# Performance work log

Measured on AMD Instinct MI355X. Metric: run time of the kernel, lower is better.

## Reference

```python
import jax, jax.numpy as jnp
import numpy as np

B, T, C = 2, 2048, 2048
H = 16
HS = C // H           # 128
ROT = HS // 2         # 64 partial-rotary dims
BASE = 10000.0


def setup_inputs() -> dict:
    key = jax.random.key(0)
    ks = jax.random.split(key, 9)
    s = 1.0 / np.sqrt(C)
    return {
        "x": jax.random.normal(ks[0], (B, T, C), jnp.float32),
        "Wq": jax.random.normal(ks[1], (C, C), jnp.float32) * s,
        "bq": jax.random.normal(ks[2], (C,), jnp.float32) * 0.02,
        "Wk": jax.random.normal(ks[3], (C, C), jnp.float32) * s,
        "bk": jax.random.normal(ks[4], (C,), jnp.float32) * 0.02,
        "Wv": jax.random.normal(ks[5], (C, C), jnp.float32) * s,
        "bv": jax.random.normal(ks[6], (C,), jnp.float32) * 0.02,
        "Wo": jax.random.normal(ks[7], (C, C), jnp.float32) * s,
        "bo": jax.random.normal(ks[8], (C,), jnp.float32) * 0.02,
    }


def _rotate_half(u):
    u1, u2 = u[..., : u.shape[-1] // 2], u[..., u.shape[-1] // 2 :]
    return jnp.concatenate((-u2, u1), axis=-1)


def _rope_tables(t_len):
    inv_freq = 1.0 / (BASE ** (jnp.arange(0, ROT, 2, dtype=jnp.float32) / ROT))
    freqs = jnp.arange(t_len, dtype=jnp.float32)[:, None] * inv_freq[None, :]
    emb = jnp.concatenate((freqs, freqs), axis=-1)  # [T, ROT]
    return jnp.cos(emb), jnp.sin(emb)


def reference(x, Wq, bq, Wk, bk, Wv, bv, Wo, bo):
    Bs, Ts, Cs = x.shape
    q = (x @ Wq.T + bq).reshape(Bs, Ts, H, HS).transpose(0, 2, 1, 3)  # [B,H,T,HS]
    k = (x @ Wk.T + bk).reshape(Bs, Ts, H, HS).transpose(0, 2, 1, 3)
    v = (x @ Wv.T + bv).reshape(Bs, Ts, H, HS).transpose(0, 2, 1, 3)

    # partial rotary on first ROT dims of each head
    cos, sin = _rope_tables(Ts)  # [T, ROT] broadcast over B,H
    q_rot, q_pass = q[..., :ROT], q[..., ROT:]
    k_rot, k_pass = k[..., :ROT], k[..., ROT:]
    q_rot = q_rot * cos + _rotate_half(q_rot) * sin
    k_rot = k_rot * cos + _rotate_half(k_rot) * sin
    q = jnp.concatenate((q_rot, q_pass), axis=-1)
    k = jnp.concatenate((k_rot, k_pass), axis=-1)

    att = jnp.einsum("bhqd,bhkd->bhqk", q, k) * (1.0 / np.sqrt(HS))
    causal = jnp.tril(jnp.ones((Ts, Ts), dtype=bool))
    att = jnp.where(causal, att, jnp.float32(-jnp.inf))
    att = jax.nn.softmax(att, axis=-1)
    out = jnp.einsum("bhqk,bhkd->bhqd", att, v)          # [B,H,T,HS]
    out = out.transpose(0, 2, 1, 3).reshape(Bs, Ts, Cs)  # [B,T,C]
    return out @ Wo.T + bo
```

## Files before the change

### kernel.cpp

```cpp
#include <hip/hip_runtime.h>
#include <hip/hip_bf16.h>

#define Bdim 2
#define Tdim 2048
#define Cdim 2048
#define Hn   16

using bf16x8 = __attribute__((ext_vector_type(8))) short;
using f32x4  = __attribute__((ext_vector_type(4))) float;
using f32x16 = __attribute__((ext_vector_type(16))) float;
typedef __hip_bfloat16 bf16;

#define VMWAIT(n) asm volatile("s_waitcnt vmcnt(" #n ")" ::: "memory")
#define CROW(r, hi) (((r) & 3) + 8 * ((r) >> 2) + 4 * (hi))
#define QS2 ((float)(0.08838834764831845 * 1.4426950408889634))
#define THR2 11.5415603f

__device__ __forceinline__ void load_lds16(const void* g, void* l) {
  __builtin_amdgcn_global_load_lds(
      (const __attribute__((address_space(1))) void*)g,
      (__attribute__((address_space(3))) void*)l, 16, 0, 0);
}

__device__ __forceinline__ float bf2f(unsigned short u) {
  union { unsigned int i; float f; } x; x.i = ((unsigned int)u) << 16; return x.f;
}
__device__ __forceinline__ unsigned short f2bf(float f) {
  bf16 h = __float2bfloat16(f); return *(unsigned short*)&h;
}
__device__ __forceinline__ unsigned cvtpk(float lo, float hi) {
  unsigned r;
  asm volatile("v_cvt_pk_bf16_f32 %0, %1, %2" : "=v"(r) : "v"(lo), "v"(hi));
  return r;
}

__global__ __launch_bounds__(256) void cvt_all(const float* __restrict__ x,
                                               const float* __restrict__ w0,
                                               const float* __restrict__ w1,
                                               const float* __restrict__ w2,
                                               const float* __restrict__ w3,
                                               bf16* __restrict__ dx,
                                               bf16* __restrict__ d0,
                                               bf16* __restrict__ d1,
                                               bf16* __restrict__ d2,
                                               bf16* __restrict__ d3) {
  const int NX = (Bdim * Tdim * Cdim) / 4;
  const int NW = (Cdim * Cdim) / 4;
  int i = blockIdx.x * 256 + threadIdx.x;
  int stride = gridDim.x * 256;
  for (; i < NX + 4 * NW; i += stride) {
    const float* s; bf16* d; int j;
    if (i < NX) { s = x; d = dx; j = i; }
    else {
      int k = i - NX;
      int wsel = k >> 20;
      j = k & (NW - 1);
      s = wsel == 0 ? w0 : wsel == 1 ? w1 : wsel == 2 ? w2 : w3;
      d = wsel == 0 ? d0 : wsel == 1 ? d1 : wsel == 2 ? d2 : d3;
    }
    float4 v = ((const float4*)s)[j];
    ushort4 o;
    o.x = f2bf(v.x); o.y = f2bf(v.y); o.z = f2bf(v.z); o.w = f2bf(v.w);
    ((ushort4*)d)[j] = o;
  }
}

__global__ __launch_bounds__(256) void rope_tables_k(float2* __restrict__ cst) {
  int idx = blockIdx.x * blockDim.x + threadIdx.x;
  if (idx >= Tdim * 32) return;
  int t = idx >> 5, i = idx & 31;
  double f = pow(10000.0, -(double)i / 32.0);
  double ang = (double)t * f;
  cst[idx] = make_float2((float)cos(ang), (float)sin(ang));
}

__global__ __launch_bounds__(512, 2) void gemmQKV(
    const bf16* __restrict__ A, const bf16* __restrict__ Wcat,
    const float* __restrict__ b0, const float* __restrict__ b1, const float* __restrict__ b2,
    bf16* __restrict__ oq, bf16* __restrict__ ok, bf16* __restrict__ vt,
    const float2* __restrict__ cst) {
  extern __shared__ char lds[];
  const int tid = threadIdx.x, lane = tid & 63, wid = tid >> 6;
  const int l31 = lane & 31, hi = lane >> 5;
  const int wr = wid >> 2, wc = wid & 3;
  const int wbase = wid * 1024;

  const int q8 = gridDim.x >> 3;
  const int swz = ((int)blockIdx.x & 7) * q8 + ((int)blockIdx.x >> 3);
  const int bm = (swz >> 4) * 256;
  const int strip = swz & 15;

  const int rS = tid >> 2, sS = tid & 3;
  const int ssw = (sS ^ ((rS >> 1) & 3)) << 3;
  const bf16* thrA = A + (size_t)(bm + rS) * 2048 + ssw;
  const bf16* thrB = Wcat + (size_t)(strip * 384 + rS) * 2048 + ssw;

#define SA(T, DB) { load_lds16(thrA + (T) * 32, (DB) + wbase);                              \
                    load_lds16(thrA + (size_t)128 * 2048 + (T) * 32, (DB) + 8192 + wbase); }
#define SB(T, DB) { load_lds16(thrB + (T) * 32, (DB) + 16384 + wbase);                      \
                    load_lds16(thrB + (size_t)128 * 2048 + (T) * 32, (DB) + 24576 + wbase); \
                    load_lds16(thrB + (size_t)256 * 2048 + (T) * 32, (DB) + 32768 + wbase); }

  f32x16 acc[4][3] = {};
  bf16x8 afr[4], bfr[3];
  const int q2 = (l31 >> 1) & 3;
  const int aoff = (wr * 128 + l31) * 64;
  const int boff = 16384 + (wc * 96 + l31) * 64;
  const int sl0 = (hi ^ q2) << 4;
  const int sl1 = sl0 ^ 32;

#define READF(PB, SL)                                                        \
  {                                                                          \
    const char* _p = (PB);                                                   \
    _Pragma("unroll")                                                        \
    for (int m_ = 0; m_ < 4; ++m_)                                           \
      afr[m_] = *(const bf16x8*)(_p + aoff + m_ * 2048 + (SL));              \
    _Pragma("unroll")                                                        \
    for (int n_ = 0; n_ < 3; ++n_)                                           \
      bfr[n_] = *(const bf16x8*)(_p + boff + n_ * 2048 + (SL));              \
  }

#define MF12()                                                               \
  __builtin_amdgcn_s_setprio(1);                                             \
  _Pragma("unroll")                                                          \
  for (int m_ = 0; m_ < 4; ++m_)                                             \
    _Pragma("unroll")                                                        \
    for (int n_ = 0; n_ < 3; ++n_)                                           \
      acc[m_][n_] = __builtin_amdgcn_mfma_f32_32x32x16_bf16(                 \
          afr[m_], bfr[n_], acc[m_][n_], 0, 0, 0);                           \
  __builtin_amdgcn_s_setprio(0);

#define BARS()                                                               \
  __builtin_amdgcn_s_barrier();                                              \
  asm volatile("s_waitcnt lgkmcnt(0)" ::: "memory");                         \
  __builtin_amdgcn_sched_barrier(0);

#define BARE() __builtin_amdgcn_s_barrier();

  SA(0, lds); SB(0, lds);
  SA(1, lds + 40960); SB(1, lds + 40960);
  VMWAIT(5);
  __builtin_amdgcn_s_barrier();

  const char* rb = lds;
  char* sb = lds + 81920;
  const int NT = 64;

  for (int t = 0; t < NT - 2; ++t) {
    READF(rb, sl0);
    SA(t + 2, sb);
    BARS(); MF12(); BARE();
    READF(rb, sl1);
    SB(t + 2, sb);
    VMWAIT(5);
    BARS(); MF12(); BARE();
    rb = (rb == lds + 81920) ? lds : rb + 40960;
    sb = (sb == lds + 81920) ? lds : sb + 40960;
  }
  {
    READF(rb, sl0);
    BARS(); MF12(); BARE();
    READF(rb, sl1);
    VMWAIT(0);
    BARS(); MF12(); BARE();
    rb = (rb == lds + 81920) ? lds : rb + 40960;
  }
  {
    READF(rb, sl0);
    BARS(); MF12(); BARE();
    READF(rb, sl1);
    BARS(); MF12(); BARE();
  }

  __syncthreads();
  if (wc == 3) {
    const int col0 = strip * 384 + 288;
    const int mat = col0 >> 11;
    if (mat < 2) {
      const int oc0 = col0 & 2047;
      const float bv = (mat == 0 ? b0 : b1)[oc0 + l31];
      #pragma unroll
      for (int m = 0; m < 4; ++m)
        #pragma unroll
        for (int g = 0; g < 4; ++g) {
          f32x4 v;
          v[0] = acc[m][0][4 * g + 0] + bv;
          v[1] = acc[m][0][4 * g + 1] + bv;
          v[2] = acc[m][0][4 * g + 2] + bv;
          v[3] = acc[m][0][4 * g + 3] + bv;
          *(f32x4*)(lds + (((((wr * 4 + m) * 4 + g) * 2 + hi) * 32) + l31) * 16) = v;
        }
    }
  }
  __syncthreads();

  #pragma unroll
  for (int m = 0; m < 4; ++m) {
    const int rowb = bm + wr * 128 + m * 32;
    const int bb = rowb >> 11, tb = rowb & 2047;
    #pragma unroll
    for (int n = 0; n < 3; ++n) {
      const int col0 = strip * 384 + wc * 96 + n * 32;
      const int mat = col0 >> 11;
      const int oc0 = col0 & 2047;
      const float bv = (mat == 0 ? b0 : mat == 1 ? b1 : b2)[oc0 + l31];
      if (mat == 2) {
        const int hh = oc0 >> 7;
        bf16* dst = vt + ((size_t)((bb * 16 + hh) * 128 + (oc0 & 127) + l31)) * 2048 + tb;
        #pragma unroll
        for (int g = 0; g < 4; ++g) {
          ushort4 pk;
          pk.x = f2bf(acc[m][n][4 * g + 0] + bv);
          pk.y = f2bf(acc[m][n][4 * g + 1] + bv);
          pk.z = f2bf(acc[m][n][4 * g + 2] + bv);
          pk.w = f2bf(acc[m][n][4 * g + 3] + bv);
          *(ushort4*)(dst + g * 8 + hi * 4) = pk;
        }
      } else {
        const float qs = (mat == 0) ? QS2 : 1.0f;
        bf16* obf = (mat == 0) ? oq : ok;
        const int hb = (wc * 3 + n) & 3;
        if (hb == 0) {
          if (wc == 2 && n == 2) {
            #pragma unroll
            for (int g = 0; g < 4; ++g) {
              f32x4 ux = *(const f32x4*)(lds + (((((wr * 4 + m) * 4 + g) * 2 + hi) * 32) + l31) * 16);
              #pragma unroll
              for (int j = 0; j < 4; ++j) {
                const int r = 4 * g + j;
                const int row = rowb + j + 8 * g + 4 * hi;
                const int tt = row & 2047;
                float2 cs = cst[tt * 32 + l31];
                float u0 = acc[m][n][r] + bv;
                float u1 = ux[j];
                obf[(size_t)row * 2048 + oc0 + l31] =
                    __float2bfloat16((u0 * cs.x - u1 * cs.y) * qs);
                obf[(size_t)row * 2048 + oc0 + 32 + l31] =
                    __float2bfloat16((u1 * cs.x + u0 * cs.y) * qs);
              }
            }
          } else {
            const float bv1 = (mat == 0 ? b0 : b1)[oc0 + 32 + l31];
            #pragma unroll
            for (int r = 0; r < 16; ++r) {
              const int row = rowb + (r & 3) + 8 * (r >> 2) + 4 * hi;
              const int tt = row & 2047;
              float2 cs = cst[tt * 32 + l31];
              float u0 = acc[m][n][r] + bv;
              float u1 = acc[m][n + 1][r] + bv1;
              obf[(size_t)row * 2048 + oc0 + l31] =
                  __float2bfloat16((u0 * cs.x - u1 * cs.y) * qs);
              obf[(size_t)row * 2048 + oc0 + 32 + l31] =
                  __float2bfloat16((u1 * cs.x + u0 * cs.y) * qs);
            }
          }
        } else if (hb >= 2) {
          #pragma unroll
          for (int r = 0; r < 16; ++r) {
            const int row = rowb + (r & 3) + 8 * (r >> 2) + 4 * hi;
            obf[(size_t)row * 2048 + oc0 + l31] =
                __float2bfloat16((acc[m][n][r] + bv) * qs);
          }
        }
      }
    }
  }
#undef SA
#undef SB
#undef READF
#undef MF12
#undef BARS
#undef BARE
}

__global__ __launch_bounds__(512, 2) void gemmWo(
    const bf16* __restrict__ A, const bf16* __restrict__ W0,
    const float* __restrict__ b0, float* __restrict__ out, int K, int nby) {
  extern __shared__ char lds[];
  const int tid = threadIdx.x, lane = tid & 63, wid = tid >> 6;
  const int l15 = lane & 15, lhi = lane >> 4;
  const int wr = wid >> 2, wc = wid & 3;
  const int fb = (wc & 1) | ((wc >> 1) << 2);

  const int q8 = gridDim.x >> 3;
  const int swz = ((int)blockIdx.x & 7) * q8 + ((int)blockIdx.x >> 3);
  const int bm = (swz / nby) * 128, bn = (swz % nby) * 256;
  const bf16* Asrc = A + (size_t)bm * K;
  const bf16* Wsrc = W0 + (size_t)bn * K;

  const bf16 *sA0, *sA1, *sB00, *sB01, *sB10, *sB11;
  {
    int c = tid, r = c >> 3, sl = c & 7;
    size_t off = (size_t)r * K + ((sl ^ (r & 7)) << 3);
    sA0 = Asrc + off;
    sA1 = Asrc + (size_t)64 * K + off;
    sB00 = Wsrc + off;
    sB10 = Wsrc + (size_t)128 * K + off;
  }
  {
    int c = 512 + tid, r = c >> 3, sl = c & 7;
    size_t off = (size_t)r * K + ((sl ^ (r & 7)) << 3);
    sB01 = Wsrc + off;
    sB11 = Wsrc + (size_t)128 * K + off;
  }
  const int ldsA = wid * 1024;

#define SA0(t) load_lds16(sA0 + (t) * 64, lds + ((t) & 1) * 49152 + ldsA)
#define SA1(t) load_lds16(sA1 + (t) * 64, lds + ((t) & 1) * 49152 + 8192 + ldsA)
#define SB0(t) { load_lds16(sB00 + (t) * 64, lds + ((t) & 1) * 49152 + 16384 + ldsA); \
                 load_lds16(sB01 + (t) * 64, lds + ((t) & 1) * 49152 + 24576 + ldsA); }
#define SB1(t) { load_lds16(sB10 + (t) * 64, lds + ((t) & 1) * 49152 + 32768 + ldsA); \
                 load_lds16(sB11 + (t) * 64, lds + ((t) & 1) * 49152 + 40960 + ldsA); }

  f32x4 acc[4][4] = {};
  const int NT = K / 64;
  const int NI = NT / 2;
  const int asw = (l15 & 7) << 4;
  bf16x8 afr[2][2], bfr0[2][2], bfr1[2][2];

#define READ_A(BASE)                                                            \
  _Pragma("unroll")                                                             \
  for (int ii = 0; ii < 2; ++ii)                                                \
    _Pragma("unroll")                                                           \
    for (int kk = 0; kk < 2; ++kk)                                              \
      afr[ii][kk] = *(const bf16x8*)((BASE) + (wr * 32 + ii * 16 + l15) * 128   \
                                     + ((kk * 64 + lhi * 16) ^ asw));

#define READ_B(BASE, DST)                                                       \
  _Pragma("unroll")                                                             \
  for (int j = 0; j < 2; ++j)                                                   \
    _Pragma("unroll")                                                           \
    for (int kk = 0; kk < 2; ++kk)                                              \
      DST[j][kk] = *(const bf16x8*)((BASE) + ((fb + 2 * j) * 16 + l15) * 128    \
                                    + ((kk * 64 + lhi * 16) ^ asw));

#define MFMA_Q(MH, NH, BF)                                                      \
  __builtin_amdgcn_s_setprio(1);                                                \
  _Pragma("unroll")                                                             \
  for (int ii = 0; ii < 2; ++ii)                                                \
    _Pragma("unroll")                                                           \
    for (int j = 0; j < 2; ++j)                                                 \
      _Pragma("unroll")                                                         \
      for (int kk = 0; kk < 2; ++kk)                                            \
        acc[(MH) * 2 + ii][(NH) * 2 + j] =                                      \
            __builtin_amdgcn_mfma_f32_16x16x32_bf16(                            \
                afr[ii][kk], BF[j][kk], acc[(MH) * 2 + ii][(NH) * 2 + j], 0, 0, 0); \
  __builtin_amdgcn_s_setprio(0);

#define BAR_IN()                                                                \
  __builtin_amdgcn_s_barrier();                                                 \
  asm volatile("s_waitcnt lgkmcnt(0)" ::: "memory");                            \
  __builtin_amdgcn_sched_barrier(0);

#define BAR_OUT() __builtin_amdgcn_s_barrier();

  SA0(0); SB0(0); SB1(0); SA1(0);
  SA0(1); SB0(1); SB1(1);
  VMWAIT(5);
  __builtin_amdgcn_s_barrier();

  char* const buf0 = lds;
  char* const buf1 = lds + 49152;

  for (int i = 0; i < NI; ++i) {
    const int t0 = 2 * i, t1 = t0 + 1;
    const bool lastI = (i == NI - 1);

    READ_A(buf0);
    READ_B(buf0 + 16384, bfr0);
    SA1(t1);
    BAR_IN(); MFMA_Q(0, 0, bfr0); BAR_OUT();

    READ_B(buf0 + 32768, bfr1);
    if (!lastI) SA0(t0 + 2);
    BAR_IN(); MFMA_Q(0, 1, bfr1); BAR_OUT();

    READ_A(buf0 + 8192);
    if (!lastI) SB0(t0 + 2);
    BAR_IN(); MFMA_Q(1, 0, bfr0); BAR_OUT();

    if (!lastI) { SB1(t0 + 2); VMWAIT(5); } else VMWAIT(0);
    BAR_IN(); MFMA_Q(1, 1, bfr1); BAR_OUT();

    READ_A(buf1);
    READ_B(buf1 + 16384, bfr0);
    if (!lastI) SA1(t0 + 2);
    BAR_IN(); MFMA_Q(0, 0, bfr0); BAR_OUT();

    READ_B(buf1 + 32768, bfr1);
    if (!lastI) SA0(t1 + 2);
    BAR_IN(); MFMA_Q(0, 1, bfr1); BAR_OUT();

    READ_A(buf1 + 8192);
    if (!lastI) SB0(t1 + 2);
    BAR_IN(); MFMA_Q(1, 0, bfr0); BAR_OUT();

    if (!lastI) { SB1(t1 + 2); VMWAIT(5); }
    BAR_IN(); MFMA_Q(1, 1, bfr1); BAR_OUT();
  }

  #pragma unroll
  for (int mi = 0; mi < 4; ++mi) {
    const int row = bm + (mi >> 1) * 64 + wr * 32 + (mi & 1) * 16 + lhi * 4;
    #pragma unroll
    for (int nj = 0; nj < 4; ++nj) {
      const int col = bn + (nj >> 1) * 128 + (fb + 2 * (nj & 1)) * 16 + l15;
      const float bv = b0[col];
      #pragma unroll
      for (int r = 0; r < 4; ++r)
        out[(size_t)(row + r) * 2048 + col] = acc[mi][nj][r] + bv;
    }
  }
#undef SA0
#undef SA1
#undef SB0
#undef SB1
#undef READ_A
#undef READ_B
#undef MFMA_Q
#undef BAR_IN
#undef BAR_OUT
}

__global__ __launch_bounds__(256, 2) void attn_kernel(const bf16* __restrict__ Q,
                                                      const bf16* __restrict__ Kb,
                                                      const bf16* __restrict__ Vt,
                                                      bf16* __restrict__ O) {
  extern __shared__ char lds[];
  const int tid = threadIdx.x, lane = tid & 63, wave = tid >> 6;
  const int l31 = lane & 31, hi = lane >> 5;
  const int hi16 = hi << 4;

  const int bid = blockIdx.x;
  const int half = bid >> 8;
  const int idx = bid & 255;
  const int g = idx >> 5;
  const int qt = half ? g : (15 - g);
  const int bh = idx & 31;
  const int b = bh >> 4, h = bh & 15;
  const size_t bT = (size_t)b * Tdim;

  const int qb = qt * 128 + wave * 32;
  const int myq = qb + l31;

  bf16x8 qf[8];
  {
    const bf16* qrow = Q + (bT + myq) * Cdim + h * 128;
    #pragma unroll
    for (int ds = 0; ds < 8; ++ds)
      qf[ds] = *(const bf16x8*)(qrow + ds * 16 + hi * 8);
  }

  auto stageKV = [&](int kt) {
    const int k0 = kt * 64;
    char* kb = lds + (kt & 1) * 16384;
    char* vb = lds + 32768 + (kt & 1) * 16384;
    #pragma unroll
    for (int i = 0; i < 4; ++i) {
      int cb = i * 256 + wave * 64;
      int c = cb + lane;
      {
        int row = c >> 4, slot = c & 15;
        load_lds16(Kb + (bT + k0 + row) * Cdim + h * 128 + ((slot ^ (row & 7)) << 3),
                   kb + cb * 16);
      }
      {
        int row = c >> 3, slot = c & 7;
        load_lds16(Vt + ((size_t)(bh * 128 + row)) * Tdim + k0 + ((slot ^ (row & 7)) << 3),
                   vb + cb * 16);
      }
    }
  };

  f32x16 o[4] = {};
  float mrun = -1e30f, lrun = 0.f;

  const int nt = 2 * (qt + 1);
  stageKV(0);

  for (int kt = 0; kt < nt; ++kt) {
    if (kt + 1 < nt) { stageKV(kt + 1); VMWAIT(8); } else { VMWAIT(0); }
    __syncthreads();
    const char* kbuf = lds + (kt & 1) * 16384;
    const char* vbuf = lds + 32768 + (kt & 1) * 16384;
    const int k0 = kt * 64;

    const bool active = (k0 <= qb + 31);
    if (active) {
      f32x16 s0 = {}, s1 = {};
      const int krow0 = l31, krow1 = 32 + l31;
      const int ksw = (l31 & 7) << 4;
      __builtin_amdgcn_s_setprio(1);
      #pragma unroll
      for (int ds = 0; ds < 8; ++ds) {
        const int boff = (ds * 32 + hi16) ^ ksw;
        bf16x8 kf0 = *(const bf16x8*)(kbuf + krow0 * 256 + boff);
        bf16x8 kf1 = *(const bf16x8*)(kbuf + krow1 * 256 + boff);
        s0 = __builtin_amdgcn_mfma_f32_32x32x16_bf16(kf0, qf[ds], s0, 0, 0, 0);
        s1 = __builtin_amdgcn_mfma_f32_32x32x16_bf16(kf1, qf[ds], s1, 0, 0, 0);
      }
      __builtin_amdgcn_s_setprio(0);

      if (k0 + 63 > qb) {
        #pragma unroll
        for (int r = 0; r < 16; ++r) {
          const int key = k0 + CROW(r, hi);
          if (key > myq)      s0[r] = -1e30f;
          if (key + 32 > myq) s1[r] = -1e30f;
        }
      }

      float mx = s0[0];
      #pragma unroll
      for (int r = 1; r < 16; ++r) mx = fmaxf(mx, s0[r]);
      #pragma unroll
      for (int r = 0; r < 16; ++r) mx = fmaxf(mx, s1[r]);
      mx = fmaxf(mx, __shfl_xor(mx, 32));
      if (!__all(mx <= mrun + THR2)) {
        const float mnew = fmaxf(mrun, mx);
        const float scl = __builtin_amdgcn_exp2f(mrun - mnew);
        lrun *= scl;
        #pragma unroll
        for (int r = 0; r < 16; ++r) {
          const float sr = __shfl(scl, CROW(r, hi));
          o[0][r] *= sr; o[1][r] *= sr; o[2][r] *= sr; o[3][r] *= sr;
        }
        mrun = mnew;
      }
      float p0[16], p1[16];
      float ps = 0.f;
      #pragma unroll
      for (int r = 0; r < 16; ++r) {
        p0[r] = __builtin_amdgcn_exp2f(s0[r] - mrun); ps += p0[r];
        p1[r] = __builtin_amdgcn_exp2f(s1[r] - mrun); ps += p1[r];
      }
      ps += __shfl_xor(ps, 32);
      lrun += ps;

      unsigned u0[8], u1[8];
      #pragma unroll
      for (int gg = 0; gg < 4; ++gg) {
        u0[gg * 2 + 0] = cvtpk(p0[gg * 4 + 0], p0[gg * 4 + 1]);
        u0[gg * 2 + 1] = cvtpk(p0[gg * 4 + 2], p0[gg * 4 + 3]);
        u1[gg * 2 + 0] = cvtpk(p1[gg * 4 + 0], p1[gg * 4 + 1]);
        u1[gg * 2 + 1] = cvtpk(p1[gg * 4 + 2], p1[gg * 4 + 3]);
      }
      bf16x8 paf[4];
      #pragma unroll
      for (int s = 0; s < 2; ++s) {
        const unsigned* us = s ? u1 : u0;
        #pragma unroll
        for (int gp = 0; gp < 2; ++gp) {
          unsigned snd0 = hi ? us[4 * gp + 0] : us[4 * gp + 2];
          unsigned snd1 = hi ? us[4 * gp + 1] : us[4 * gp + 3];
          unsigned rcv0 = __shfl_xor((int)snd0, 32);
          unsigned rcv1 = __shfl_xor((int)snd1, 32);
          union { unsigned w[4]; bf16x8 v; } fr;
          if (hi == 0) {
            fr.w[0] = us[4 * gp + 0]; fr.w[1] = us[4 * gp + 1];
            fr.w[2] = rcv0;           fr.w[3] = rcv1;
          } else {
            fr.w[0] = rcv0;           fr.w[1] = rcv1;
            fr.w[2] = us[4 * gp + 2]; fr.w[3] = us[4 * gp + 3];
          }
          paf[s * 2 + gp] = fr.v;
        }
      }

      __builtin_amdgcn_s_setprio(1);
      #pragma unroll
      for (int dblk = 0; dblk < 4; ++dblk) {
        const int d = dblk * 32 + l31;
        const int vswz = (d & 7) << 4;
        #pragma unroll
        for (int ks = 0; ks < 4; ++ks) {
          bf16x8 vf = *(const bf16x8*)(vbuf + d * 128 + ((ks * 32 + hi16) ^ vswz));
          o[dblk] = __builtin_amdgcn_mfma_f32_32x32x16_bf16(paf[ks], vf, o[dblk], 0, 0, 0);
        }
      }
      __builtin_amdgcn_s_setprio(0);
    }
    __syncthreads();
  }

  const float inv = 1.f / lrun;
  #pragma unroll
  for (int r = 0; r < 16; ++r) {
    const float ir = __shfl(inv, CROW(r, hi));
    const int qrow = qb + CROW(r, hi);
    bf16* orow = O + (bT + qrow) * Cdim + h * 128;
    #pragma unroll
    for (int dblk = 0; dblk < 4; ++dblk)
      orow[dblk * 32 + l31] = __float2bfloat16(o[dblk][r] * ir);
  }
}

extern "C" void kernel_launch(void* const* d_in, const int* in_sizes, int n_in,
                              void* d_out, int out_size, void* d_ws, size_t ws_size,
                              hipStream_t stream) {
  const float* x  = (const float*)d_in[0];
  const float* Wq = (const float*)d_in[1];
  const float* bq = (const float*)d_in[2];
  const float* Wk = (const float*)d_in[3];
  const float* bk = (const float*)d_in[4];
  const float* Wv = (const float*)d_in[5];
  const float* bv = (const float*)d_in[6];
  const float* Wo = (const float*)d_in[7];
  const float* bo = (const float*)d_in[8];

  char* ws = (char*)d_ws;
  const size_t SZ_X  = (size_t)Bdim * Tdim * Cdim * 2;
  const size_t SZ_W  = (size_t)Cdim * Cdim * 2;
  bf16* x_bf  = (bf16*)(ws);
  bf16* Wq_bf = (bf16*)(ws + SZ_X);
  bf16* Wk_bf = (bf16*)(ws + SZ_X + SZ_W);
  bf16* Wv_bf = (bf16*)(ws + SZ_X + 2 * SZ_W);
  bf16* Wo_bf = (bf16*)(ws + SZ_X + 3 * SZ_W);
  bf16* q_bf  = (bf16*)(ws + SZ_X + 4 * SZ_W);
  bf16* k_bf  = (bf16*)(ws + 2 * SZ_X + 4 * SZ_W);
  bf16* v_t   = (bf16*)(ws + 3 * SZ_X + 4 * SZ_W);
  bf16* a_bf  = (bf16*)(ws + 4 * SZ_X + 4 * SZ_W);
  float2* cst = (float2*)(ws + 5 * SZ_X + 4 * SZ_W);

  const int K = Cdim;

  rope_tables_k<<<(Tdim * 32 + 255) / 256, 256, 0, stream>>>(cst);
  cvt_all<<<2048, 256, 0, stream>>>(x, Wq, Wk, Wv, Wo,
                                    x_bf, Wq_bf, Wk_bf, Wv_bf, Wo_bf);

  gemmQKV<<<256, 512, 122880, stream>>>(
      x_bf, Wq_bf, bq, bk, bv, q_bf, k_bf, v_t, cst);

  attn_kernel<<<512, 256, 65536, stream>>>(q_bf, k_bf, v_t, a_bf);

  gemmWo<<<256, 512, 98304, stream>>>(
      a_bf, Wo_bf, bo, (float*)d_out, K, 8);
}
```

Measured before the change: 231.0 us.

## Double-buffer register fragments and drop per-half barriers in QKV GEMM mainloop

Restructures the QKV projection GEMM main loop so LDS fragment reads for the next k-half go into a second register set while the current half's MFMAs run. Partial lgkmcnt waits replace full drains, and the four barriers per tile become one. Global-to-LDS prefetch of both A and B tiles is issued after that single barrier, with a full vmcnt(0) wait. This aims to hide LDS latency and cut barrier stalls, at the cost of doubling fragment registers and waiting on global loads more strictly.

```diff
diff --git a/kernel.cpp b/kernel.cpp
--- a/kernel.cpp
+++ b/kernel.cpp
@@ -102,74 +102,82 @@
                     load_lds16(thrB + (size_t)256 * 2048 + (T) * 32, (DB) + 32768 + wbase); }
 
   f32x16 acc[4][3] = {};
-  bf16x8 afr[4], bfr[3];
+  bf16x8 afr0[4], bfr0[3], afr1[4], bfr1[3];
   const int q2 = (l31 >> 1) & 3;
   const int aoff = (wr * 128 + l31) * 64;
   const int boff = 16384 + (wc * 96 + l31) * 64;
   const int sl0 = (hi ^ q2) << 4;
   const int sl1 = sl0 ^ 32;
 
-#define READF(PB, SL)                                                        \
+#define READF(AF, BF, PB, SL)                                                \
   {                                                                          \
     const char* _p = (PB);                                                   \
     _Pragma("unroll")                                                        \
     for (int m_ = 0; m_ < 4; ++m_)                                           \
-      afr[m_] = *(const bf16x8*)(_p + aoff + m_ * 2048 + (SL));              \
+      AF[m_] = *(const bf16x8*)(_p + aoff + m_ * 2048 + (SL));               \
     _Pragma("unroll")                                                        \
     for (int n_ = 0; n_ < 3; ++n_)                                           \
-      bfr[n_] = *(const bf16x8*)(_p + boff + n_ * 2048 + (SL));              \
-  }
-
-#define MF12()                                                               \
+      BF[n_] = *(const bf16x8*)(_p + boff + n_ * 2048 + (SL));               \
+  }
+
+#define MF12(AF, BF)                                                         \
   __builtin_amdgcn_s_setprio(1);                                             \
   _Pragma("unroll")                                                          \
   for (int m_ = 0; m_ < 4; ++m_)                                             \
     _Pragma("unroll")                                                        \
     for (int n_ = 0; n_ < 3; ++n_)                                           \
       acc[m_][n_] = __builtin_amdgcn_mfma_f32_32x32x16_bf16(                 \
-          afr[m_], bfr[n_], acc[m_][n_], 0, 0, 0);                           \
+          AF[m_], BF[n_], acc[m_][n_], 0, 0, 0);                             \
   __builtin_amdgcn_s_setprio(0);
 
-#define BARS()                                                               \
-  __builtin_amdgcn_s_barrier();                                              \
-  asm volatile("s_waitcnt lgkmcnt(0)" ::: "memory");                         \
+#define LGK7()                                                               \
+  asm volatile("s_waitcnt lgkmcnt(7)" ::: "memory");                         \
   __builtin_amdgcn_sched_barrier(0);
-
-#define BARE() __builtin_amdgcn_s_barrier();
 
   SA(0, lds); SB(0, lds);
   SA(1, lds + 40960); SB(1, lds + 40960);
   VMWAIT(5);
   __builtin_amdgcn_s_barrier();
+  __builtin_amdgcn_sched_barrier(0);
+  READF(afr0, bfr0, lds, sl0);
 
   const char* rb = lds;
+  const char* nb = lds + 40960;
   char* sb = lds + 81920;
   const int NT = 64;
 
   for (int t = 0; t < NT - 2; ++t) {
-    READF(rb, sl0);
-    SA(t + 2, sb);
-    BARS(); MF12(); BARE();
-    READF(rb, sl1);
-    SB(t + 2, sb);
-    VMWAIT(5);
-    BARS(); MF12(); BARE();
-    rb = (rb == lds + 81920) ? lds : rb + 40960;
-    sb = (sb == lds + 81920) ? lds : sb + 40960;
+    READF(afr1, bfr1, rb, sl1);
+    LGK7();
+    MF12(afr0, bfr0);
+    VMWAIT(0);
+    __builtin_amdgcn_s_barrier();
+    __builtin_amdgcn_sched_barrier(0);
+    SA(t + 2, sb); SB(t + 2, sb);
+    READF(afr0, bfr0, nb, sl0);
+    LGK7();
+    MF12(afr1, bfr1);
+    char* old = (char*)rb; rb = nb; nb = sb; sb = old;
   }
   {
-    READF(rb, sl0);
-    BARS(); MF12(); BARE();
-    READF(rb, sl1);
+    READF(afr1, bfr1, rb, sl1);
+    LGK7();
+    MF12(afr0, bfr0);
     VMWAIT(0);
-    BARS(); MF12(); BARE();
-    rb = (rb == lds + 81920) ? lds : rb + 40960;
+    __builtin_amdgcn_s_barrier();
+    __builtin_amdgcn_sched_barrier(0);
+    READF(afr0, bfr0, nb, sl0);
+    LGK7();
+    MF12(afr1, bfr1);
+    rb = nb;
   }
   {
-    READF(rb, sl0);
-    BARS(); MF12(); BARE();
-    READF(rb, sl1);
-    BARS(); MF12(); BARE();
+    READF(afr1, bfr1, rb, sl1);
+    LGK7();
+    MF12(afr0, bfr0);
+    asm volatile("s_waitcnt lgkmcnt(0)" ::: "memory");
+    __builtin_amdgcn_sched_barrier(0);
+    MF12(afr1, bfr1);
   }
 
   __syncthreads();
@@ -269,8 +277,7 @@
 #undef SB
 #undef READF
 #undef MF12
-#undef BARS
-#undef BARE
+#undef LGK7
 }
 
 __global__ __launch_bounds__(512, 2) void gemmWo(
```

Result: slower. 275.8 us (+19.4%).

## Restructure QKV GEMM main loop to one barrier per K-tile with fragment prefetch

Applied to the files above, without the earlier changes.

The projection GEMM's K loop used to synchronise four times per tile (two barrier pairs, each with an lgkmcnt wait). It now uses a single barrier per tile, issued after waiting for all outstanding global-to-LDS loads. After that barrier it issues the next tile's global loads and prefetches the first LDS fragment of the next buffer into registers. This cuts barrier and wait overhead and lets MFMA work run back to back. In exchange, the full vmcnt(0) wait reduces how far global loads can overlap with compute, and the fragment registers are reused while MFMAs may still be consuming them.

```diff
diff --git a/kernel.cpp b/kernel.cpp
--- a/kernel.cpp
+++ b/kernel.cpp
@@ -130,46 +130,43 @@
           afr[m_], bfr[n_], acc[m_][n_], 0, 0, 0);                           \
   __builtin_amdgcn_s_setprio(0);
 
-#define BARS()                                                               \
-  __builtin_amdgcn_s_barrier();                                              \
-  asm volatile("s_waitcnt lgkmcnt(0)" ::: "memory");                         \
-  __builtin_amdgcn_sched_barrier(0);
-
-#define BARE() __builtin_amdgcn_s_barrier();
-
   SA(0, lds); SB(0, lds);
   SA(1, lds + 40960); SB(1, lds + 40960);
   VMWAIT(5);
   __builtin_amdgcn_s_barrier();
+  __builtin_amdgcn_sched_barrier(0);
+  READF(lds, sl0);
 
   const char* rb = lds;
+  const char* nb = lds + 40960;
   char* sb = lds + 81920;
   const int NT = 64;
 
   for (int t = 0; t < NT - 2; ++t) {
-    READF(rb, sl0);
-    SA(t + 2, sb);
-    BARS(); MF12(); BARE();
+    MF12();
     READF(rb, sl1);
-    SB(t + 2, sb);
-    VMWAIT(5);
-    BARS(); MF12(); BARE();
-    rb = (rb == lds + 81920) ? lds : rb + 40960;
-    sb = (sb == lds + 81920) ? lds : sb + 40960;
+    MF12();
+    VMWAIT(0);
+    __builtin_amdgcn_s_barrier();
+    __builtin_amdgcn_sched_barrier(0);
+    SA(t + 2, sb); SB(t + 2, sb);
+    READF(nb, sl0);
+    char* old = (char*)rb; rb = nb; nb = sb; sb = old;
   }
   {
-    READF(rb, sl0);
-    BARS(); MF12(); BARE();
+    MF12();
     READF(rb, sl1);
+    MF12();
     VMWAIT(0);
-    BARS(); MF12(); BARE();
-    rb = (rb == lds + 81920) ? lds : rb + 40960;
+    __builtin_amdgcn_s_barrier();
+    __builtin_amdgcn_sched_barrier(0);
+    READF(nb, sl0);
+    rb = nb;
   }
   {
-    READF(rb, sl0);
-    BARS(); MF12(); BARE();
+    MF12();
     READF(rb, sl1);
-    BARS(); MF12(); BARE();
+    MF12();
   }
 
   __syncthreads();
@@ -269,8 +266,6 @@
 #undef SB
 #undef READF
 #undef MF12
-#undef BARS
-#undef BARE
 }
 
 __global__ __launch_bounds__(512, 2) void gemmWo(
```

Result: no change. 231.3 us (+0.1%).
